# Kernel optimization log

Measured on AMD Instinct MI355X. Metric: run time of the kernel, lower is better.

The kernel has to match this reference:

```python
import jax, jax.numpy as jnp
import numpy as np

N_NODES, N_EDGES = 10000, 160000
LATENT, N_EXP, N_SPECIES = 128, 8, 16
AVG_NEIGH = 16.0
EPS = 1e-8
# irreps: 64x0e + 32x1e + 16x2e -> flat dim 64 + 32*3 + 16*5 = 240

def _split(x):
    return x[:, :64], x[:, 64:160].reshape(-1, 32, 3), x[:, 160:240].reshape(-1, 16, 5)

def _merge(s, v, t):
    return jnp.concatenate([s, v.reshape(v.shape[0], -1), t.reshape(t.shape[0], -1)], axis=-1)

def _sep_ln(x, g, b):
    # separable layer norm: LN on scalars, per-degree component RMS norm on l>0
    s, v, t = _split(x)
    s = (s - s.mean(-1, keepdims=True)) * jax.lax.rsqrt(s.var(-1, keepdims=True) + EPS) * g[:64] + b
    v = v * jax.lax.rsqrt((v * v).mean((1, 2), keepdims=True) + EPS) * g[64:96][None, :, None]
    t = t * jax.lax.rsqrt((t * t).mean((1, 2), keepdims=True) + EPS) * g[96:112][None, :, None]
    return _merge(s, v, t)

def _forward(latents, node_features, edge_features, node_onehot, edge_vector,
             ln_gn, ln_bn, ln_ge, ln_be, Wg, W0, W1, W2, P0, b0, P1, P2,
             Wenv, benv, T0, T1, T2, edge_index):
    ec, en = edge_index[0], edge_index[1]
    nf_n = _sep_ln(node_features, ln_gn, ln_bn)
    ef_n = _sep_ln(edge_features, ln_ge, ln_be)
    # gather center/neighbor node features per edge (irregular access)
    c0, c1, c2 = _split(nf_n[ec])
    n0, n1, n2 = _split(nf_n[en])
    e0, e1, e2 = _split(ef_n)
    in0 = jnp.concatenate([c0, e0, n0], -1)   # [E,192]
    in1 = jnp.concatenate([c1, e1, n1], 1)    # [E,96,3]
    in2 = jnp.concatenate([c2, e2, n2], 1)    # [E,48,5]
    # latent-conditioned MoE tensor product: per-l linear with expert-mixed weights
    gates = jax.nn.softmax(latents @ Wg, axis=-1)            # [E,K]
    out0 = jnp.einsum('ek,kio,ei->eo', gates, W0, in0)        # [E,112]
    out1 = jnp.einsum('ek,kio,eim->eom', gates, W1, in1)      # [E,32,3]
    out2 = jnp.einsum('ek,kio,eim->eom', gates, W2, in2)      # [E,16,5]
    # gated nonlinearity: silu scalars, sigmoid gates multiply l>0 blocks
    s = jax.nn.silu(out0[:, :64])
    g1 = jax.nn.sigmoid(out0[:, 64:96])
    g2 = jax.nn.sigmoid(out0[:, 96:112])
    v = out1 * g1[:, :, None]
    t = out2 * g2[:, :, None]
    # lin_post (per-degree linear, bias on scalars)
    s = s @ P0 + b0
    v = jnp.einsum('eim,io->eom', v, P1)
    t = jnp.einsum('eim,io->eom', t, P2)
    # env element-wise weighting from latents (E3ElementLinear)
    w = latents @ Wenv + benv                                 # [E,112]
    msg = _merge(s * w[:, :64], v * w[:, 64:96, None], t * w[:, 96:112, None])
    # scatter-aggregate to center nodes
    agg = jax.ops.segment_sum(msg, ec, num_segments=node_features.shape[0])
    new_nf = agg * (AVG_NEIGH ** -0.5)
    # residual update with logit-parametrized ratio (param=0 -> u=0.5)
    u = jax.nn.sigmoid(jnp.zeros((), new_nf.dtype))
    c_old = jax.lax.rsqrt(u * u + 1.0)
    c_new = u * c_old
    nf = c_old * node_features + c_new * new_nf
    # species one-hot fully-connected TP correction
    s2, v2, t2 = _split(nf)
    ds = jnp.einsum('ni,nk,iko->no', s2, node_onehot, T0)
    dv = jnp.einsum('nim,nk,iko->nom', v2, node_onehot, T1)
    dt = jnp.einsum('nim,nk,iko->nom', t2, node_onehot, T2)
    return nf + _merge(ds, dv, dt)

def setup_inputs():
    key = jax.random.key(0)
    ks = jax.random.split(key, 20)
    f32 = jnp.float32
    return {
        'latents': jax.random.normal(ks[0], (N_EDGES, LATENT), f32),
        'node_features': jax.random.normal(ks[1], (N_NODES, 240), f32),
        'edge_features': jax.random.normal(ks[2], (N_EDGES, 240), f32),
        'node_onehot': jax.nn.one_hot(jax.random.randint(ks[3], (N_NODES,), 0, N_SPECIES), N_SPECIES, dtype=f32),
        'edge_vector': jax.random.normal(ks[4], (N_EDGES, 3), f32),
        'ln_gn': jnp.ones((112,), f32), 'ln_bn': jnp.zeros((64,), f32),
        'ln_ge': jnp.ones((112,), f32), 'ln_be': jnp.zeros((64,), f32),
        'Wg': jax.random.normal(ks[5], (LATENT, N_EXP), f32) * 0.1,
        'W0': jax.random.normal(ks[6], (N_EXP, 192, 112), f32) / float(np.sqrt(192)),
        'W1': jax.random.normal(ks[7], (N_EXP, 96, 32), f32) / float(np.sqrt(96)),
        'W2': jax.random.normal(ks[8], (N_EXP, 48, 16), f32) / float(np.sqrt(48)),
        'P0': jax.random.normal(ks[9], (64, 64), f32) / 8.0,
        'b0': jnp.zeros((64,), f32),
        'P1': jax.random.normal(ks[10], (32, 32), f32) / float(np.sqrt(32)),
        'P2': jax.random.normal(ks[11], (16, 16), f32) / 4.0,
        'Wenv': jax.random.normal(ks[12], (LATENT, 112), f32) / float(np.sqrt(LATENT)),
        'benv': jnp.zeros((112,), f32),
        'T0': jax.random.normal(ks[13], (64, N_SPECIES, 64), f32) / float(np.sqrt(64 * N_SPECIES)),
        'T1': jax.random.normal(ks[14], (32, N_SPECIES, 32), f32) / float(np.sqrt(32 * N_SPECIES)),
        'T2': jax.random.normal(ks[15], (16, N_SPECIES, 16), f32) / float(np.sqrt(16 * N_SPECIES)),
        'edge_index': jax.random.randint(ks[16], (2, N_EDGES), 0, N_NODES),
    }

def reference(latents, node_features, edge_features, node_onehot, edge_vector,
              ln_gn, ln_bn, ln_ge, ln_be, Wg, W0, W1, W2, P0, b0, P1, P2,
              Wenv, benv, T0, T1, T2, edge_index):
    return _forward(latents, node_features, edge_features, node_onehot, edge_vector,
                    ln_gn, ln_bn, ln_ge, ln_be, Wg, W0, W1, W2, P0, b0, P1, P2,
                    Wenv, benv, T0, T1, T2, edge_index)
```

## Files before the change

### kernel.cpp

```cpp
#include <hip/hip_runtime.h>
#include <math.h>

#define N_NODES 10000
#define N_EDGES 160000
#define EPS 1e-8f

typedef __attribute__((ext_vector_type(8))) __bf16 bf16x8;
typedef __attribute__((ext_vector_type(4))) float f32x4;

__device__ __forceinline__ f32x4 MFMA(bf16x8 a, bf16x8 b, f32x4 c){
  return __builtin_amdgcn_mfma_f32_16x16x32_bf16(a, b, c, 0, 0, 0);
}

__device__ __forceinline__ float wave_sum64(float x) {
  #pragma unroll
  for (int m = 32; m >= 1; m >>= 1) x += __shfl_xor(x, m, 64);
  return x;
}
__device__ __forceinline__ float gsum16(float x) {
  x += __shfl_xor(x, 1, 64); x += __shfl_xor(x, 2, 64);
  x += __shfl_xor(x, 4, 64); x += __shfl_xor(x, 8, 64);
  return x;
}

#define X0O 0
#define X1O 6144
#define X2O 15360
#define O0O 0
#define O1O 6144
#define O2O 15360
#define WvO 21760
#define SMEM_BYTES 52352

#define W0O 0
#define W1O 196608
#define W2O 221184
#define WEO 229376
#define P0O 245760
#define P1O 249856
#define P2O 250880
#define WTOT 251392

__device__ __forceinline__ void prep_seg(int u, const float* __restrict__ src,
                                         __bf16* __restrict__ dst,
                                         int NT, int KS, int Ka, int Na) {
  int per = NT * KS * 512;
  int e = u / per; int r = u - e * per;
  int nt = r / (KS * 512); r -= nt * KS * 512;
  int ks = r >> 9; int li = r & 511;
  int lane = li >> 3, j = li & 7;
  int k = ks * 32 + ((lane >> 4) << 3) + j;
  int n = nt * 16 + (lane & 15);
  float v = (k < Ka && n < Na) ? src[((size_t)e * Ka + k) * Na + n] : 0.f;
  dst[u] = (__bf16)v;
}

__global__ __launch_bounds__(256)
void k_prep(const float* __restrict__ W0, const float* __restrict__ W1,
            const float* __restrict__ W2, const float* __restrict__ We,
            const float* __restrict__ P0, const float* __restrict__ P1,
            const float* __restrict__ P2, __bf16* __restrict__ dst) {
  int t = blockIdx.x * 256 + threadIdx.x;
  if (t >= WTOT) return;
  if      (t < W1O) prep_seg(t - W0O, W0, dst + W0O, 8, 6, 192, 112);
  else if (t < W2O) prep_seg(t - W1O, W1, dst + W1O, 2, 3,  96,  32);
  else if (t < WEO) prep_seg(t - W2O, W2, dst + W2O, 1, 2,  48,  16);
  else if (t < P0O) prep_seg(t - WEO, We, dst + WEO, 8, 4, 128, 112);
  else if (t < P1O) prep_seg(t - P0O, P0, dst + P0O, 4, 2,  64,  64);
  else if (t < P2O) prep_seg(t - P1O, P1, dst + P1O, 2, 1,  32,  32);
  else              prep_seg(t - P2O, P2, dst + P2O, 1, 1,  16,  16);
}

__global__ __launch_bounds__(256)
void k_node_ln(const float* __restrict__ nf, const float* __restrict__ gn,
               const float* __restrict__ bn, __bf16* __restrict__ nfn) {
  int node = blockIdx.x * 4 + (threadIdx.x >> 6);
  int lane = threadIdx.x & 63;
  const float* row = nf + (size_t)node * 240;
  __bf16* out = nfn + (size_t)node * 240;
  float s = row[lane];
  float mean = wave_sum64(s) * (1.f / 64.f);
  float d = s - mean;
  float var = wave_sum64(d * d) * (1.f / 64.f);
  float rstd = rsqrtf(var + EPS);
  out[lane] = (__bf16)(d * rstd * gn[lane] + bn[lane]);
  float v0 = row[64 + lane];
  float v1 = (lane < 32) ? row[128 + lane] : 0.f;
  float rsv = rsqrtf(wave_sum64(v0 * v0 + v1 * v1) * (1.f / 96.f) + EPS);
  { int vi = lane; int i = vi / 3, m = vi - 3 * i;
    out[64 + m * 32 + i] = (__bf16)(v0 * rsv * gn[64 + i]); }
  if (lane < 32) { int vi = 64 + lane; int i = vi / 3, m = vi - 3 * i;
    out[64 + m * 32 + i] = (__bf16)(v1 * rsv * gn[64 + i]); }
  float t0 = row[160 + lane];
  float t1 = (lane < 16) ? row[224 + lane] : 0.f;
  float rst = rsqrtf(wave_sum64(t0 * t0 + t1 * t1) * (1.f / 80.f) + EPS);
  { int ti = lane; int i = ti / 5, m = ti - 5 * i;
    out[160 + m * 16 + i] = (__bf16)(t0 * rst * gn[96 + i]); }
  if (lane < 16) { int ti = 64 + lane; int i = ti / 5, m = ti - 5 * i;
    out[160 + m * 16 + i] = (__bf16)(t1 * rst * gn[96 + i]); }
}

__global__ __launch_bounds__(256)
void k_stats(const float* __restrict__ ef, float4* __restrict__ stats) {
  int row = blockIdx.x * 4 + (threadIdx.x >> 6);
  int lane = threadIdx.x & 63;
  const float* r = ef + (size_t)row * 240;
  float s = r[lane];
  float mean = wave_sum64(s) * (1.f / 64.f);
  float d = s - mean;
  float var = wave_sum64(d * d) * (1.f / 64.f);
  float rstd = rsqrtf(var + EPS);
  float v0 = r[64 + lane];
  float v1 = (lane < 32) ? r[128 + lane] : 0.f;
  float rsv = rsqrtf(wave_sum64(v0 * v0 + v1 * v1) * (1.f / 96.f) + EPS);
  float t0 = r[160 + lane];
  float t1 = (lane < 16) ? r[224 + lane] : 0.f;
  float rst = rsqrtf(wave_sum64(t0 * t0 + t1 * t1) * (1.f / 80.f) + EPS);
  if (lane == 0) stats[row] = make_float4(mean, rstd, rsv, rst);
}

__global__ __launch_bounds__(256)
void k_gate(const float* __restrict__ latents, const float* __restrict__ Wg,
            float* __restrict__ gatesG) {
  int row = blockIdx.x * 16 + (threadIdx.x >> 4);
  int sl = threadIdx.x & 15;
  const float* lrow = latents + (size_t)row * 128 + sl * 8;
  float4 u4 = *(const float4*)lrow;
  float4 w4 = *(const float4*)(lrow + 4);
  float lv[8] = {u4.x, u4.y, u4.z, u4.w, w4.x, w4.y, w4.z, w4.w};
  float ga[8] = {};
  #pragma unroll
  for (int dd = 0; dd < 8; ++dd) {
    const float* wgr = Wg + (sl * 8 + dd) * 8;
    #pragma unroll
    for (int k = 0; k < 8; ++k) ga[k] += lv[dd] * wgr[k];
  }
  #pragma unroll
  for (int k = 0; k < 8; ++k) ga[k] = gsum16(ga[k]);
  float mx = ga[0];
  #pragma unroll
  for (int k = 1; k < 8; ++k) mx = fmaxf(mx, ga[k]);
  float den = 0.f;
  #pragma unroll
  for (int k = 0; k < 8; ++k) { ga[k] = expf(ga[k] - mx); den += ga[k]; }
  float val = 0.f;
  #pragma unroll
  for (int k = 0; k < 8; ++k) if (sl == k) val = ga[k];
  if (sl < 8) gatesG[(size_t)row * 8 + sl] = val / den;
}

__global__ __launch_bounds__(512, 4)
void k_edge(const float* __restrict__ latents, const float* __restrict__ ef,
            const __bf16* __restrict__ nfn, const int* __restrict__ eidx,
            const float* __restrict__ ln_ge, const float* __restrict__ ln_be,
            const float4* __restrict__ stats, const float* __restrict__ gatesG,
            const __bf16* __restrict__ Wsw,
            const float* __restrict__ pb0, const float* __restrict__ benv,
            float* __restrict__ agg) {
  __shared__ __align__(16) char smem[SMEM_BYTES];
  float* gatesL = (float*)(smem + 51200);
  int* ecsL = (int*)(smem + 52224);
  __bf16* SBF = (__bf16*)smem;

  const int tid = threadIdx.x;
  const int e0 = blockIdx.x * 32;
  const int w = tid >> 6, lane = tid & 63, kg = lane >> 4, l16 = lane & 15;
  const int eg = tid >> 4, sl = tid & 15;
  const int xsw = (eg & 7) << 4;
  const int xswr = (l16 & 7) << 4;

  const int ec = eidx[e0 + eg], en = eidx[N_EDGES + e0 + eg];
  if (tid < 32) ecsL[tid] = eidx[e0 + tid];
  if (tid < 256) gatesL[tid] = gatesG[(size_t)e0 * 8 + tid];
  uint2 cvr[4], nvr[4]; float4 evf[4];
  #pragma unroll
  for (int j = 0; j < 4; ++j) {
    int ch = j * 16 + sl;
    if (ch < 60) {
      int p = ch * 4;
      cvr[j] = *(const uint2*)(nfn + (size_t)ec * 240 + p);
      nvr[j] = *(const uint2*)(nfn + (size_t)en * 240 + p);
      evf[j] = *(const float4*)(ef + (size_t)(e0 + eg) * 240 + p);
    }
  }
  float4 st = stats[e0 + eg];

  {
    #pragma unroll
    for (int j = 0; j < 4; ++j) {
      int ch = j * 16 + sl;
      if (ch < 60) {
        int p = ch * 4;
        float e4[4] = {evf[j].x, evf[j].y, evf[j].z, evf[j].w};
        if (p < 64) {
          int off = X0O + eg * 192;
          *(uint2*)(smem + (((off + p) * 2) ^ xsw)) = cvr[j];
          *(uint2*)(smem + (((off + 128 + p) * 2) ^ xsw)) = nvr[j];
          __bf16 eb[4];
          #pragma unroll
          for (int t = 0; t < 4; ++t) {
            int c = p + t;
            eb[t] = (__bf16)((e4[t] - st.x) * st.y * ln_ge[c] + ln_be[c]);
          }
          *(uint2*)(smem + (((off + 64 + p) * 2) ^ xsw)) = *(uint2*)eb;
        } else if (p < 160) {
          int q = p - 64;
          int m = q >> 5, i = q & 31;
          int off = X1O + (m * 32 + eg) * 96;
          *(uint2*)(smem + (((off + i) * 2) ^ xsw)) = cvr[j];
          *(uint2*)(smem + (((off + 64 + i) * 2) ^ xsw)) = nvr[j];
          #pragma unroll
          for (int t = 0; t < 4; ++t) {
            int k = q + t; int ei = k / 3, em = k - 3 * ei;
            float y = e4[t] * st.z * ln_ge[64 + ei];
            *(__bf16*)(smem + (((X1O + (em * 32 + eg) * 96 + 32 + ei) * 2) ^ xsw)) = (__bf16)y;
          }
        } else {
          int q = p - 160;
          int m = q >> 4, i = q & 15;
          int off = X2O + (m * 32 + eg) * 64;
          *(uint2*)(smem + (((off + i) * 2) ^ xsw)) = cvr[j];
          *(uint2*)(smem + (((off + 32 + i) * 2) ^ xsw)) = nvr[j];
          #pragma unroll
          for (int t = 0; t < 4; ++t) {
            int k = q + t; int ei = k / 5, em = k - 5 * ei;
            float y = e4[t] * st.w * ln_ge[96 + ei];
            *(__bf16*)(smem + (((X2O + (em * 32 + eg) * 64 + 16 + ei) * 2) ^ xsw)) = (__bf16)y;
          }
        }
      }
    }
    for (int z = tid; z < 640; z += 512) {
      int r = z >> 2, c4 = (z & 3) * 4;
      uint2 zz; zz.x = 0; zz.y = 0;
      *(uint2*)(smem + (((X2O + r * 64 + 48 + c4) * 2) ^ ((r & 7) << 4))) = zz;
    }
  }
  __syncthreads();

  {
    const int mt = w & 1, ntA = (w >> 1) * 2;
    f32x4 acc[2] = {};
    const __bf16* WB = Wsw + W0O;
    for (int ex = 0; ex < 8; ++ex) {
      f32x4 D[2] = {};
      #pragma unroll
      for (int ks = 0; ks < 6; ++ks) {
        bf16x8 a = *(const bf16x8*)(smem + (((X0O + (mt * 16 + l16) * 192 + ks * 32 + kg * 8) * 2) ^ xswr));
        bf16x8 bA = *(const bf16x8*)(WB + (((ex * 8 + ntA) * 6 + ks) << 9) + lane * 8);
        bf16x8 bB = *(const bf16x8*)(WB + (((ex * 8 + ntA + 1) * 6 + ks) << 9) + lane * 8);
        D[0] = MFMA(a, bA, D[0]); D[1] = MFMA(a, bB, D[1]);
      }
      #pragma unroll
      for (int jj = 0; jj < 4; ++jj) {
        float g = gatesL[(mt * 16 + kg * 4 + jj) * 8 + ex];
        acc[0][jj] += g * D[0][jj]; acc[1][jj] += g * D[1][jj];
      }
    }
    __syncthreads();
    #pragma unroll
    for (int ni = 0; ni < 2; ++ni) {
      int cc = (ntA + ni) * 16 + l16;
      if (cc < 112)
        #pragma unroll
        for (int jj = 0; jj < 4; ++jj) {
          float x = acc[ni][jj];
          float sg = 1.f / (1.f + expf(-x));
          float val = (cc < 64) ? x * sg : sg;
          SBF[O0O + (mt * 16 + kg * 4 + jj) * 120 + cc] = (__bf16)val;
        }
    }
  }

  const int nu1 = (w < 4) ? 2 : 1;
  const int mtv0 = w >> 1, ntv = w & 1, mtv1 = (w >> 1) + 4;
  {
    f32x4 acc[2] = {};
    const __bf16* WB = Wsw + W1O;
    for (int ex = 0; ex < 8; ++ex) {
      f32x4 D[2] = {};
      #pragma unroll
      for (int ks = 0; ks < 3; ++ks) {
        bf16x8 b = *(const bf16x8*)(WB + (((ex * 2 + ntv) * 3 + ks) << 9) + lane * 8);
        bf16x8 a0 = *(const bf16x8*)(smem + (((X1O + (mtv0 * 16 + l16) * 96 + ks * 32 + kg * 8) * 2) ^ xswr));
        D[0] = MFMA(a0, b, D[0]);
        if (nu1 == 2) {
          bf16x8 a1 = *(const bf16x8*)(smem + (((X1O + (mtv1 * 16 + l16) * 96 + ks * 32 + kg * 8) * 2) ^ xswr));
          D[1] = MFMA(a1, b, D[1]);
        }
      }
      #pragma unroll
      for (int jj = 0; jj < 4; ++jj) {
        int r0 = mtv0 * 16 + kg * 4 + jj;
        acc[0][jj] += gatesL[(r0 & 31) * 8 + ex] * D[0][jj];
        if (nu1 == 2) {
          int r1 = mtv1 * 16 + kg * 4 + jj;
          acc[1][jj] += gatesL[(r1 & 31) * 8 + ex] * D[1][jj];
        }
      }
    }
    __syncthreads();
    const int o = ntv * 16 + l16;
    #pragma unroll
    for (int jj = 0; jj < 4; ++jj) {
      int r0 = mtv0 * 16 + kg * 4 + jj;
      float g0 = (float)SBF[O0O + (r0 & 31) * 120 + 64 + o];
      SBF[O1O + r0 * 40 + o] = (__bf16)(acc[0][jj] * g0);
      if (nu1 == 2) {
        int r1 = mtv1 * 16 + kg * 4 + jj;
        float g1 = (float)SBF[O0O + (r1 & 31) * 120 + 64 + o];
        SBF[O1O + r1 * 40 + o] = (__bf16)(acc[1][jj] * g1);
      }
    }
  }

  const int nu2 = (w < 2) ? 2 : 1;
  const int mt20 = w, mt21 = w + 8;
  {
    f32x4 acc[2] = {};
    const __bf16* WB = Wsw + W2O;
    for (int ex = 0; ex < 8; ++ex) {
      f32x4 D[2] = {};
      #pragma unroll
      for (int ks = 0; ks < 2; ++ks) {
        bf16x8 b = *(const bf16x8*)(WB + ((ex * 2 + ks) << 9) + lane * 8);
        bf16x8 a0 = *(const bf16x8*)(smem + (((X2O + (mt20 * 16 + l16) * 64 + ks * 32 + kg * 8) * 2) ^ xswr));
        D[0] = MFMA(a0, b, D[0]);
        if (nu2 == 2) {
          bf16x8 a1 = *(const bf16x8*)(smem + (((X2O + (mt21 * 16 + l16) * 64 + ks * 32 + kg * 8) * 2) ^ xswr));
          D[1] = MFMA(a1, b, D[1]);
        }
      }
      #pragma unroll
      for (int jj = 0; jj < 4; ++jj) {
        int r0 = mt20 * 16 + kg * 4 + jj;
        acc[0][jj] += gatesL[(r0 & 31) * 8 + ex] * D[0][jj];
        if (nu2 == 2) {
          int r1 = mt21 * 16 + kg * 4 + jj;
          acc[1][jj] += gatesL[(r1 & 31) * 8 + ex] * D[1][jj];
        }
      }
    }
    __syncthreads();
    #pragma unroll
    for (int jj = 0; jj < 4; ++jj) {
      int r0 = mt20 * 16 + kg * 4 + jj;
      float g0 = (float)SBF[O0O + (r0 & 31) * 120 + 96 + l16];
      SBF[O2O + r0 * 40 + l16] = (__bf16)(acc[0][jj] * g0);
      SBF[O2O + r0 * 40 + 16 + l16] = (__bf16)0.f;
      if (nu2 == 2) {
        int r1 = mt21 * 16 + kg * 4 + jj;
        float g1 = (float)SBF[O0O + (r1 & 31) * 120 + 96 + l16];
        SBF[O2O + r1 * 40 + l16] = (__bf16)(acc[1][jj] * g1);
        SBF[O2O + r1 * 40 + 16 + l16] = (__bf16)0.f;
      }
    }
  }

  {
    const int mt = w >> 2, np = (w & 3) * 2;
    f32x4 acc[2] = {};
    const __bf16* WB = Wsw + WEO;
    #pragma unroll
    for (int ks = 0; ks < 4; ++ks) {
      bf16x8 a;
      const float* lp = latents + (size_t)(e0 + mt * 16 + l16) * 128 + ks * 32 + kg * 8;
      float4 u4 = *(const float4*)lp; float4 v4 = *(const float4*)(lp + 4);
      a[0]=(__bf16)u4.x; a[1]=(__bf16)u4.y; a[2]=(__bf16)u4.z; a[3]=(__bf16)u4.w;
      a[4]=(__bf16)v4.x; a[5]=(__bf16)v4.y; a[6]=(__bf16)v4.z; a[7]=(__bf16)v4.w;
      bf16x8 bA = *(const bf16x8*)(WB + ((np * 4 + ks) << 9) + lane * 8);
      bf16x8 bB = *(const bf16x8*)(WB + (((np + 1) * 4 + ks) << 9) + lane * 8);
      acc[0] = MFMA(a, bA, acc[0]); acc[1] = MFMA(a, bB, acc[1]);
    }
    #pragma unroll
    for (int ni = 0; ni < 2; ++ni) {
      int cc = (np + ni) * 16 + l16;
      if (cc < 112) {
        float bv = benv[cc];
        #pragma unroll
        for (int jj = 0; jj < 4; ++jj)
          SBF[WvO + (mt * 16 + kg * 4 + jj) * 120 + cc] = (__bf16)(acc[ni][jj] + bv);
      }
    }
  }
  __syncthreads();

  {
    const int mt = w & 1, nt = w >> 1;
    f32x4 ps = {};
    const __bf16* WB = Wsw + P0O;
    #pragma unroll
    for (int ks = 0; ks < 2; ++ks) {
      bf16x8 a = *(const bf16x8*)(SBF + O0O + (mt * 16 + l16) * 120 + ks * 32 + kg * 8);
      bf16x8 b = *(const bf16x8*)(WB + ((nt * 2 + ks) << 9) + lane * 8);
      ps = MFMA(a, b, ps);
    }
    int cc = nt * 16 + l16;
    float bias = pb0[cc];
    #pragma unroll
    for (int jj = 0; jj < 4; ++jj) {
      int row = mt * 16 + kg * 4 + jj;
      float msg = (ps[jj] + bias) * (float)SBF[WvO + row * 120 + cc];
      atomicAdd(&agg[(size_t)ecsL[row] * 240 + cc], msg);
    }
  }
  {
    f32x4 pv[2] = {};
    const __bf16* WB = Wsw + P1O;
    bf16x8 b = *(const bf16x8*)(WB + (ntv << 9) + lane * 8);
    bf16x8 a0 = *(const bf16x8*)(SBF + O1O + (mtv0 * 16 + l16) * 40 + kg * 8);
    pv[0] = MFMA(a0, b, pv[0]);
    if (nu1 == 2) {
      bf16x8 a1 = *(const bf16x8*)(SBF + O1O + (mtv1 * 16 + l16) * 40 + kg * 8);
      pv[1] = MFMA(a1, b, pv[1]);
    }
    const int o = ntv * 16 + l16;
    #pragma unroll
    for (int jj = 0; jj < 4; ++jj) {
      int r0 = mtv0 * 16 + kg * 4 + jj;
      int m = r0 >> 5, eL = r0 & 31;
      float msg = pv[0][jj] * (float)SBF[WvO + eL * 120 + 64 + o];
      atomicAdd(&agg[(size_t)ecsL[eL] * 240 + 64 + m * 32 + o], msg);
      if (nu1 == 2) {
        int r1 = mtv1 * 16 + kg * 4 + jj;
        int m1 = r1 >> 5, eL1 = r1 & 31;
        float msg1 = pv[1][jj] * (float)SBF[WvO + eL1 * 120 + 64 + o];
        atomicAdd(&agg[(size_t)ecsL[eL1] * 240 + 64 + m1 * 32 + o], msg1);
      }
    }
  }
  {
    f32x4 pt[2] = {};
    const __bf16* WB = Wsw + P2O;
    bf16x8 b = *(const bf16x8*)(WB + lane * 8);
    bf16x8 a0 = *(const bf16x8*)(SBF + O2O + (mt20 * 16 + l16) * 40 + kg * 8);
    pt[0] = MFMA(a0, b, pt[0]);
    if (nu2 == 2) {
      bf16x8 a1 = *(const bf16x8*)(SBF + O2O + (mt21 * 16 + l16) * 40 + kg * 8);
      pt[1] = MFMA(a1, b, pt[1]);
    }
    const int o = l16;
    #pragma unroll
    for (int jj = 0; jj < 4; ++jj) {
      int r0 = mt20 * 16 + kg * 4 + jj;
      int m = r0 >> 5, eL = r0 & 31;
      float msg = pt[0][jj] * (float)SBF[WvO + eL * 120 + 96 + o];
      atomicAdd(&agg[(size_t)ecsL[eL] * 240 + 160 + m * 16 + o], msg);
      if (nu2 == 2) {
        int r1 = mt21 * 16 + kg * 4 + jj;
        int m1 = r1 >> 5, eL1 = r1 & 31;
        float msg1 = pt[1][jj] * (float)SBF[WvO + eL1 * 120 + 96 + o];
        atomicAdd(&agg[(size_t)ecsL[eL1] * 240 + 160 + m1 * 16 + o], msg1);
      }
    }
  }
}

__global__ __launch_bounds__(256)
void k_node(const float* __restrict__ nf, const float* __restrict__ agg,
            const float* __restrict__ onehot, const float* __restrict__ T0,
            const float* __restrict__ T1, const float* __restrict__ T2,
            float* __restrict__ out) {
  int w = threadIdx.x >> 6;
  int lane = threadIdx.x & 63;
  int node = blockIdx.x * 4 + w;
  __shared__ float buf[4][240];
  const float* nrow = nf + (size_t)node * 240;
  const float* arow = agg + (size_t)node * 240;
  const float c_old = 0.894427190999916f;
  const float c_new_s = 0.447213595499958f * 0.25f;
  for (int j = lane; j < 240; j += 64) {
    int src;
    if (j < 64) src = j;
    else if (j < 160) { int vi = j - 64; int o = vi / 3, m = vi - 3 * o; src = 64 + m * 32 + o; }
    else              { int ti = j - 160; int o = ti / 5, m = ti - 5 * o; src = 160 + m * 16 + o; }
    buf[w][j] = c_old * nrow[j] + c_new_s * arow[src];
  }
  float ohv = (lane < 16) ? onehot[(size_t)node * 16 + lane] : 0.f;
  unsigned long long msk = __ballot(ohv > 0.5f);
  int kk = __ffsll((unsigned long long)msk) - 1;
  __syncthreads();
  #pragma unroll
  for (int rep = 0; rep < 4; ++rep) {
    int c = rep * 64 + lane;
    if (c >= 240) break;
    float d;
    if (c < 64) {
      const float* tp = T0 + (size_t)kk * 64 + c;
      float a = 0.f;
      for (int i = 0; i < 64; ++i) a = fmaf(buf[w][i], tp[(size_t)i * 1024], a);
      d = a;
    } else if (c < 160) {
      int vi = c - 64; int o = vi / 3, m = vi - o * 3;
      const float* tp = T1 + (size_t)kk * 32 + o;
      float a = 0.f;
      for (int i = 0; i < 32; ++i) a = fmaf(buf[w][64 + i * 3 + m], tp[(size_t)i * 512], a);
      d = a;
    } else {
      int ti = c - 160; int o = ti / 5, m = ti - o * 5;
      const float* tp = T2 + (size_t)kk * 16 + o;
      float a = 0.f;
      for (int i = 0; i < 16; ++i) a = fmaf(buf[w][160 + i * 5 + m], tp[(size_t)i * 256], a);
      d = a;
    }
    out[(size_t)node * 240 + c] = buf[w][c] + d;
  }
}

extern "C" void kernel_launch(void* const* d_in, const int* in_sizes, int n_in,
                              void* d_out, int out_size, void* d_ws, size_t ws_size,
                              hipStream_t stream) {
  (void)in_sizes; (void)n_in; (void)out_size; (void)ws_size;
  const float* latents       = (const float*)d_in[0];
  const float* node_features = (const float*)d_in[1];
  const float* edge_features = (const float*)d_in[2];
  const float* node_onehot   = (const float*)d_in[3];
  const float* ln_gn = (const float*)d_in[5];
  const float* ln_bn = (const float*)d_in[6];
  const float* ln_ge = (const float*)d_in[7];
  const float* ln_be = (const float*)d_in[8];
  const float* Wg    = (const float*)d_in[9];
  const float* W0    = (const float*)d_in[10];
  const float* W1    = (const float*)d_in[11];
  const float* W2    = (const float*)d_in[12];
  const float* P0    = (const float*)d_in[13];
  const float* b0    = (const float*)d_in[14];
  const float* P1    = (const float*)d_in[15];
  const float* P2    = (const float*)d_in[16];
  const float* Wenv  = (const float*)d_in[17];
  const float* benv  = (const float*)d_in[18];
  const float* T0    = (const float*)d_in[19];
  const float* T1    = (const float*)d_in[20];
  const float* T2    = (const float*)d_in[21];
  const int*   eidx  = (const int*)d_in[22];
  float* out = (float*)d_out;

  __bf16* nfn    = (__bf16*)d_ws;
  float*  agg    = (float*)((char*)d_ws + 4800000);
  __bf16* Wsw    = (__bf16*)((char*)d_ws + 14400000);
  float4* stats  = (float4*)((char*)d_ws + 15000000);
  float*  gatesG = (float*)((char*)d_ws + 17600000);

  hipMemsetAsync(agg, 0, 2400000 * sizeof(float), stream);
  k_prep<<<(WTOT + 255) / 256, 256, 0, stream>>>(W0, W1, W2, Wenv, P0, P1, P2, Wsw);
  k_node_ln<<<N_NODES / 4, 256, 0, stream>>>(node_features, ln_gn, ln_bn, nfn);
  k_stats<<<N_EDGES / 4, 256, 0, stream>>>(edge_features, stats);
  k_gate<<<N_EDGES / 16, 256, 0, stream>>>(latents, Wg, gatesG);
  k_edge<<<N_EDGES / 32, 512, 0, stream>>>(latents, edge_features, nfn, eidx,
      ln_ge, ln_be, stats, gatesG, Wsw, b0, benv, agg);
  k_node<<<N_NODES / 4, 256, 0, stream>>>(node_features, agg, node_onehot, T0, T1, T2, out);
}
```

Measured before the change: 536.8 us.

## Fuse node LN, edge stats and gating into one kernel; retile scalar MoE GEMM

Merges the node layer-norm, edge-feature statistics and gate softmax kernels into a single launch, with the gate computed per edge by a full wave in the same block that computes that edge's stats. This removes two launches and their tail effects. The scalar MoE GEMM is retiled so each wave owns one N-tile across both M-tiles, sharing the weight fragment across two MFMAs instead of sharing the A fragment. s_setprio is raised around the three MoE MFMA loops. The gate now uses full 64-lane reductions, which adds shuffle work per edge.

```diff
diff --git a/kernel.cpp b/kernel.cpp
--- a/kernel.cpp
+++ b/kernel.cpp
@@ -15,11 +15,6 @@
 __device__ __forceinline__ float wave_sum64(float x) {
   #pragma unroll
   for (int m = 32; m >= 1; m >>= 1) x += __shfl_xor(x, m, 64);
-  return x;
-}
-__device__ __forceinline__ float gsum16(float x) {
-  x += __shfl_xor(x, 1, 64); x += __shfl_xor(x, 2, 64);
-  x += __shfl_xor(x, 4, 64); x += __shfl_xor(x, 8, 64);
   return x;
 }
 
@@ -72,81 +67,71 @@
 }
 
 __global__ __launch_bounds__(256)
-void k_node_ln(const float* __restrict__ nf, const float* __restrict__ gn,
-               const float* __restrict__ bn, __bf16* __restrict__ nfn) {
-  int node = blockIdx.x * 4 + (threadIdx.x >> 6);
-  int lane = threadIdx.x & 63;
-  const float* row = nf + (size_t)node * 240;
-  __bf16* out = nfn + (size_t)node * 240;
-  float s = row[lane];
-  float mean = wave_sum64(s) * (1.f / 64.f);
-  float d = s - mean;
-  float var = wave_sum64(d * d) * (1.f / 64.f);
-  float rstd = rsqrtf(var + EPS);
-  out[lane] = (__bf16)(d * rstd * gn[lane] + bn[lane]);
-  float v0 = row[64 + lane];
-  float v1 = (lane < 32) ? row[128 + lane] : 0.f;
-  float rsv = rsqrtf(wave_sum64(v0 * v0 + v1 * v1) * (1.f / 96.f) + EPS);
-  { int vi = lane; int i = vi / 3, m = vi - 3 * i;
-    out[64 + m * 32 + i] = (__bf16)(v0 * rsv * gn[64 + i]); }
-  if (lane < 32) { int vi = 64 + lane; int i = vi / 3, m = vi - 3 * i;
-    out[64 + m * 32 + i] = (__bf16)(v1 * rsv * gn[64 + i]); }
-  float t0 = row[160 + lane];
-  float t1 = (lane < 16) ? row[224 + lane] : 0.f;
-  float rst = rsqrtf(wave_sum64(t0 * t0 + t1 * t1) * (1.f / 80.f) + EPS);
-  { int ti = lane; int i = ti / 5, m = ti - 5 * i;
-    out[160 + m * 16 + i] = (__bf16)(t0 * rst * gn[96 + i]); }
-  if (lane < 16) { int ti = 64 + lane; int i = ti / 5, m = ti - 5 * i;
-    out[160 + m * 16 + i] = (__bf16)(t1 * rst * gn[96 + i]); }
-}
-
-__global__ __launch_bounds__(256)
-void k_stats(const float* __restrict__ ef, float4* __restrict__ stats) {
-  int row = blockIdx.x * 4 + (threadIdx.x >> 6);
-  int lane = threadIdx.x & 63;
-  const float* r = ef + (size_t)row * 240;
-  float s = r[lane];
-  float mean = wave_sum64(s) * (1.f / 64.f);
-  float d = s - mean;
-  float var = wave_sum64(d * d) * (1.f / 64.f);
-  float rstd = rsqrtf(var + EPS);
-  float v0 = r[64 + lane];
-  float v1 = (lane < 32) ? r[128 + lane] : 0.f;
-  float rsv = rsqrtf(wave_sum64(v0 * v0 + v1 * v1) * (1.f / 96.f) + EPS);
-  float t0 = r[160 + lane];
-  float t1 = (lane < 16) ? r[224 + lane] : 0.f;
-  float rst = rsqrtf(wave_sum64(t0 * t0 + t1 * t1) * (1.f / 80.f) + EPS);
-  if (lane == 0) stats[row] = make_float4(mean, rstd, rsv, rst);
-}
-
-__global__ __launch_bounds__(256)
-void k_gate(const float* __restrict__ latents, const float* __restrict__ Wg,
-            float* __restrict__ gatesG) {
-  int row = blockIdx.x * 16 + (threadIdx.x >> 4);
-  int sl = threadIdx.x & 15;
-  const float* lrow = latents + (size_t)row * 128 + sl * 8;
-  float4 u4 = *(const float4*)lrow;
-  float4 w4 = *(const float4*)(lrow + 4);
-  float lv[8] = {u4.x, u4.y, u4.z, u4.w, w4.x, w4.y, w4.z, w4.w};
-  float ga[8] = {};
-  #pragma unroll
-  for (int dd = 0; dd < 8; ++dd) {
-    const float* wgr = Wg + (sl * 8 + dd) * 8;
-    #pragma unroll
-    for (int k = 0; k < 8; ++k) ga[k] += lv[dd] * wgr[k];
-  }
-  #pragma unroll
-  for (int k = 0; k < 8; ++k) ga[k] = gsum16(ga[k]);
-  float mx = ga[0];
-  #pragma unroll
-  for (int k = 1; k < 8; ++k) mx = fmaxf(mx, ga[k]);
-  float den = 0.f;
-  #pragma unroll
-  for (int k = 0; k < 8; ++k) { ga[k] = expf(ga[k] - mx); den += ga[k]; }
-  float val = 0.f;
-  #pragma unroll
-  for (int k = 0; k < 8; ++k) if (sl == k) val = ga[k];
-  if (sl < 8) gatesG[(size_t)row * 8 + sl] = val / den;
+void k_pre(const float* __restrict__ nf, const float* __restrict__ gn,
+           const float* __restrict__ bn, __bf16* __restrict__ nfn,
+           const float* __restrict__ ef, float4* __restrict__ stats,
+           const float* __restrict__ latents, const float* __restrict__ Wg,
+           float* __restrict__ gatesG) {
+  const int lane = threadIdx.x & 63;
+  if (blockIdx.x < 2500) {
+    int node = blockIdx.x * 4 + (threadIdx.x >> 6);
+    const float* row = nf + (size_t)node * 240;
+    __bf16* out = nfn + (size_t)node * 240;
+    float s = row[lane];
+    float mean = wave_sum64(s) * (1.f / 64.f);
+    float d = s - mean;
+    float var = wave_sum64(d * d) * (1.f / 64.f);
+    float rstd = rsqrtf(var + EPS);
+    out[lane] = (__bf16)(d * rstd * gn[lane] + bn[lane]);
+    float v0 = row[64 + lane];
+    float v1 = (lane < 32) ? row[128 + lane] : 0.f;
+    float rsv = rsqrtf(wave_sum64(v0 * v0 + v1 * v1) * (1.f / 96.f) + EPS);
+    { int vi = lane; int i = vi / 3, m = vi - 3 * i;
+      out[64 + m * 32 + i] = (__bf16)(v0 * rsv * gn[64 + i]); }
+    if (lane < 32) { int vi = 64 + lane; int i = vi / 3, m = vi - 3 * i;
+      out[64 + m * 32 + i] = (__bf16)(v1 * rsv * gn[64 + i]); }
+    float t0 = row[160 + lane];
+    float t1 = (lane < 16) ? row[224 + lane] : 0.f;
+    float rst = rsqrtf(wave_sum64(t0 * t0 + t1 * t1) * (1.f / 80.f) + EPS);
+    { int ti = lane; int i = ti / 5, m = ti - 5 * i;
+      out[160 + m * 16 + i] = (__bf16)(t0 * rst * gn[96 + i]); }
+    if (lane < 16) { int ti = 64 + lane; int i = ti / 5, m = ti - 5 * i;
+      out[160 + m * 16 + i] = (__bf16)(t1 * rst * gn[96 + i]); }
+  } else {
+    int row = (blockIdx.x - 2500) * 4 + (threadIdx.x >> 6);
+    const float* r = ef + (size_t)row * 240;
+    float s = r[lane];
+    float mean = wave_sum64(s) * (1.f / 64.f);
+    float d = s - mean;
+    float var = wave_sum64(d * d) * (1.f / 64.f);
+    float rstd = rsqrtf(var + EPS);
+    float v0 = r[64 + lane];
+    float v1 = (lane < 32) ? r[128 + lane] : 0.f;
+    float rsv = rsqrtf(wave_sum64(v0 * v0 + v1 * v1) * (1.f / 96.f) + EPS);
+    float t0 = r[160 + lane];
+    float t1 = (lane < 16) ? r[224 + lane] : 0.f;
+    float rst = rsqrtf(wave_sum64(t0 * t0 + t1 * t1) * (1.f / 80.f) + EPS);
+    if (lane == 0) stats[row] = make_float4(mean, rstd, rsv, rst);
+    const float* lrow = latents + (size_t)row * 128;
+    float lv0 = lrow[lane], lv1 = lrow[64 + lane];
+    const float* wg0 = Wg + lane * 8;
+    const float* wg1 = Wg + (64 + lane) * 8;
+    float ga[8];
+    #pragma unroll
+    for (int k = 0; k < 8; ++k) ga[k] = lv0 * wg0[k] + lv1 * wg1[k];
+    #pragma unroll
+    for (int k = 0; k < 8; ++k) ga[k] = wave_sum64(ga[k]);
+    float mx = ga[0];
+    #pragma unroll
+    for (int k = 1; k < 8; ++k) mx = fmaxf(mx, ga[k]);
+    float den = 0.f;
+    #pragma unroll
+    for (int k = 0; k < 8; ++k) { ga[k] = expf(ga[k] - mx); den += ga[k]; }
+    float val = 0.f;
+    #pragma unroll
+    for (int k = 0; k < 8; ++k) if (lane == k) val = ga[k];
+    if (lane < 8) gatesG[(size_t)row * 8 + lane] = val / den;
+  }
 }
 
 __global__ __launch_bounds__(512, 4)
@@ -239,36 +224,39 @@
   __syncthreads();
 
   {
-    const int mt = w & 1, ntA = (w >> 1) * 2;
+    const int nt = w;
     f32x4 acc[2] = {};
     const __bf16* WB = Wsw + W0O;
+    __builtin_amdgcn_s_setprio(1);
     for (int ex = 0; ex < 8; ++ex) {
       f32x4 D[2] = {};
       #pragma unroll
       for (int ks = 0; ks < 6; ++ks) {
-        bf16x8 a = *(const bf16x8*)(smem + (((X0O + (mt * 16 + l16) * 192 + ks * 32 + kg * 8) * 2) ^ xswr));
-        bf16x8 bA = *(const bf16x8*)(WB + (((ex * 8 + ntA) * 6 + ks) << 9) + lane * 8);
-        bf16x8 bB = *(const bf16x8*)(WB + (((ex * 8 + ntA + 1) * 6 + ks) << 9) + lane * 8);
-        D[0] = MFMA(a, bA, D[0]); D[1] = MFMA(a, bB, D[1]);
+        bf16x8 a0 = *(const bf16x8*)(smem + (((X0O + l16 * 192 + ks * 32 + kg * 8) * 2) ^ xswr));
+        bf16x8 a1 = *(const bf16x8*)(smem + (((X0O + (16 + l16) * 192 + ks * 32 + kg * 8) * 2) ^ xswr));
+        bf16x8 bA = *(const bf16x8*)(WB + (((ex * 8 + nt) * 6 + ks) << 9) + lane * 8);
+        D[0] = MFMA(a0, bA, D[0]); D[1] = MFMA(a1, bA, D[1]);
       }
       #pragma unroll
       for (int jj = 0; jj < 4; ++jj) {
-        float g = gatesL[(mt * 16 + kg * 4 + jj) * 8 + ex];
-        acc[0][jj] += g * D[0][jj]; acc[1][jj] += g * D[1][jj];
-      }
-    }
+        float g0 = gatesL[(kg * 4 + jj) * 8 + ex];
+        float g1 = gatesL[(16 + kg * 4 + jj) * 8 + ex];
+        acc[0][jj] += g0 * D[0][jj]; acc[1][jj] += g1 * D[1][jj];
+      }
+    }
+    __builtin_amdgcn_s_setprio(0);
     __syncthreads();
-    #pragma unroll
-    for (int ni = 0; ni < 2; ++ni) {
-      int cc = (ntA + ni) * 16 + l16;
-      if (cc < 112)
-        #pragma unroll
-        for (int jj = 0; jj < 4; ++jj) {
-          float x = acc[ni][jj];
-          float sg = 1.f / (1.f + expf(-x));
-          float val = (cc < 64) ? x * sg : sg;
-          SBF[O0O + (mt * 16 + kg * 4 + jj) * 120 + cc] = (__bf16)val;
-        }
+    int cc = nt * 16 + l16;
+    if (cc < 112) {
+      #pragma unroll
+      for (int jj = 0; jj < 4; ++jj) {
+        float x0 = acc[0][jj];
+        float sg0 = 1.f / (1.f + expf(-x0));
+        SBF[O0O + (kg * 4 + jj) * 120 + cc] = (__bf16)((cc < 64) ? x0 * sg0 : sg0);
+        float x1 = acc[1][jj];
+        float sg1 = 1.f / (1.f + expf(-x1));
+        SBF[O0O + (16 + kg * 4 + jj) * 120 + cc] = (__bf16)((cc < 64) ? x1 * sg1 : sg1);
+      }
     }
   }
 
@@ -277,6 +265,7 @@
   {
     f32x4 acc[2] = {};
     const __bf16* WB = Wsw + W1O;
+    __builtin_amdgcn_s_setprio(1);
     for (int ex = 0; ex < 8; ++ex) {
       f32x4 D[2] = {};
       #pragma unroll
@@ -299,6 +288,7 @@
         }
       }
     }
+    __builtin_amdgcn_s_setprio(0);
     __syncthreads();
     const int o = ntv * 16 + l16;
     #pragma unroll
@@ -319,6 +309,7 @@
   {
     f32x4 acc[2] = {};
     const __bf16* WB = Wsw + W2O;
+    __builtin_amdgcn_s_setprio(1);
     for (int ex = 0; ex < 8; ++ex) {
       f32x4 D[2] = {};
       #pragma unroll
@@ -341,6 +332,7 @@
         }
       }
     }
+    __builtin_amdgcn_s_setprio(0);
     __syncthreads();
     #pragma unroll
     for (int jj = 0; jj < 4; ++jj) {
@@ -543,9 +535,8 @@
 
   hipMemsetAsync(agg, 0, 2400000 * sizeof(float), stream);
   k_prep<<<(WTOT + 255) / 256, 256, 0, stream>>>(W0, W1, W2, Wenv, P0, P1, P2, Wsw);
-  k_node_ln<<<N_NODES / 4, 256, 0, stream>>>(node_features, ln_gn, ln_bn, nfn);
-  k_stats<<<N_EDGES / 4, 256, 0, stream>>>(edge_features, stats);
-  k_gate<<<N_EDGES / 16, 256, 0, stream>>>(latents, Wg, gatesG);
+  k_pre<<<2500 + 40000, 256, 0, stream>>>(node_features, ln_gn, ln_bn, nfn,
+      edge_features, stats, latents, Wg, gatesG);
   k_edge<<<N_EDGES / 32, 512, 0, stream>>>(latents, edge_features, nfn, eidx,
       ln_ge, ln_be, stats, gatesG, Wsw, b0, benv, agg);
   k_node<<<N_NODES / 4, 256, 0, stream>>>(node_features, agg, node_onehot, T0, T1, T2, out);
```

Measured after the change: 547.7 us. 2.0% more time.
